# Performance work log

Measured on AMD Instinct MI355X. Metric: run time of the kernel, lower is better.

## Reference

```python
import math
import jax, jax.numpy as jnp
import numpy as np

N, C, H, W = 32, 64, 96, 96
SHIFT_H, SHIFT_W = 1, -1  # fixed values of the random roll shifts

def _dwconv(x, w, dilation, pad):
    # depthwise conv, x: (n,c,h,w), w: (c,1,kh,kw)
    return jax.lax.conv_general_dilated(
        x, w, window_strides=(1, 1), padding=((pad, pad), (pad, pad)),
        rhs_dilation=(dilation, dilation),
        dimension_numbers=('NCHW', 'OIHW', 'NCHW'),
        feature_group_count=x.shape[1])

def _unfold_1x7_d2(x):
    # F.unfold(x, (1,7), dilation=(1,2), padding=(0,6)) -> (n,c,7,h,w)
    n, c, h, w = x.shape
    xp = jnp.pad(x, ((0, 0), (0, 0), (0, 0), (6, 6)))
    return jnp.stack([xp[..., 2 * k: 2 * k + w] for k in range(7)], axis=2)

def setup_inputs() -> dict:
    key = jax.random.key(0)
    k0, k1, k2, k3, k4, k5 = jax.random.split(key, 6)
    std = 0.1
    return {
        'x':  jax.random.normal(k0, (N, C, H, W), dtype=jnp.float32),
        'w3': jax.random.normal(k1, (C, 1, 5, 5), dtype=jnp.float32) * std,
        'w4': jax.random.normal(k2, (C, 1, 3, 3), dtype=jnp.float32) * std,
        'p5': jax.random.normal(k3, (1, C, C), dtype=jnp.float32) * std,
        'p6': jax.random.normal(k4, (C, 1), dtype=jnp.float32) * std,
        'p8': jax.random.normal(k5, (C, C * 7), dtype=jnp.float32) * std,
    }

def reference(x, w3, w4, p5, p6, p8):
    n, c, h, w = x.shape
    hw = h * w
    t0 = x
    t1 = jnp.roll(jnp.roll(t0, SHIFT_H, axis=2), SHIFT_W, axis=3)
    # channel attention: (n,c,c)
    t2 = jnp.einsum('nci,ndi->ncd', t0.reshape(n, c, hw), t1.reshape(n, c, hw)) / math.sqrt(hw)
    t3 = _dwconv(t1, w3, dilation=1, pad=2)          # (n,c,h,w)
    t4 = _dwconv(t1, w4, dilation=2, pad=2)          # (n,c,h,w)
    t5 = p5 * t2                                      # (n,c,c)
    t6 = jnp.einsum('nchw,ce->nehw', t4, p6).reshape(n, h, w)
    t7 = _unfold_1x7_d2(t0).reshape(n, c * 7, hw)     # (n, c*7, hw)
    t8 = jnp.einsum('nbc,bd->ndc', t5, p8)            # (n, c*7, c)
    t9 = jnp.einsum('nci,ni->nc', t3.reshape(n, c, hw), t6.reshape(n, hw)) / math.sqrt(hw)
    t10 = jnp.einsum('nkc,nks->ncs', t8, t7) / math.sqrt(c * 7)  # (n,c,hw)
    t11 = t9[:, :, None] + t10
    return t11.reshape(n, c, h, w)
```

## Files before the change

### kernel.cpp

```cpp
#include <hip/hip_runtime.h>

#define NB 32
#define CCH 64
#define HH 96
#define WWID 96
#define HWP (HH*WWID)
#define K7 448

#define OFF_T5 2097152
#define OFF_T8 2228224
#define OFF_T6 3145728
#define OFF_T9 3440640

typedef __attribute__((ext_vector_type(8))) short short8;
typedef __attribute__((ext_vector_type(4))) float floatx4;

__device__ __forceinline__ short f2bf(float x) {
    unsigned u = __float_as_uint(x);
    unsigned r = (u + 0x7FFF + ((u >> 16) & 1)) >> 16;
    return (short)r;
}

__device__ __forceinline__ int roll_idx(int i) {
    int h = i / WWID;
    int w = i - h * WWID;
    return ((h + HH - 1) % HH) * WWID + ((w + 1) % WWID);
}

__global__ __launch_bounds__(256) void k_t2(const float* __restrict__ x,
                                            float* __restrict__ t2p) {
    int blk = blockIdx.x;
    int n = blk >> 4, sl = blk & 15;
    int k0 = sl * (HWP / 16);
    __shared__ float ash[32][68];
    __shared__ float bsh[32][68];
    int t = threadIdx.x;
    int c0 = (t >> 4) * 4;
    int d0 = (t & 15) * 4;
    float acc[4][4] = {};
    const float* xa = x + (size_t)n * CCH * HWP;

    for (int kc = 0; kc < 576; kc += 32) {
        __syncthreads();
#pragma unroll
        for (int i = 0; i < 8; i++) {
            int idx = i * 256 + t;
            int c = idx >> 5, kk = idx & 31;
            int gi = k0 + kc + kk;
            ash[kk][c] = xa[c * HWP + gi];
            bsh[kk][c] = xa[c * HWP + roll_idx(gi)];
        }
        __syncthreads();
#pragma unroll
        for (int kk = 0; kk < 32; kk++) {
            float4 va = *(const float4*)&ash[kk][c0];
            float4 vb = *(const float4*)&bsh[kk][d0];
            float av[4] = {va.x, va.y, va.z, va.w};
            float bv[4] = {vb.x, vb.y, vb.z, vb.w};
#pragma unroll
            for (int i = 0; i < 4; i++)
#pragma unroll
                for (int j = 0; j < 4; j++)
                    acc[i][j] = fmaf(av[i], bv[j], acc[i][j]);
        }
    }
    float* o = t2p + (((size_t)n * 16 + sl) * 64 + c0) * 64 + d0;
#pragma unroll
    for (int i = 0; i < 4; i++) {
        float4 v = {acc[i][0], acc[i][1], acc[i][2], acc[i][3]};
        *(float4*)(o + i * 64) = v;
    }
}

__global__ __launch_bounds__(256) void k_t5(const float* __restrict__ t2p,
                                            const float* __restrict__ p5,
                                            float* __restrict__ t5) {
    int idx = blockIdx.x * 256 + threadIdx.x;
    int n = idx >> 12, rc = idx & 4095;
    float s = 0.f;
#pragma unroll
    for (int sl = 0; sl < 16; sl++)
        s += t2p[((size_t)n * 16 + sl) * 4096 + rc];
    t5[idx] = s * p5[rc] * (1.0f / 96.0f);
}

__global__ __launch_bounds__(256) void k_t8(const float* __restrict__ t5,
                                            const float* __restrict__ p8,
                                            short* __restrict__ t8t) {
    int n = blockIdx.y;
    int idx = blockIdx.x * 256 + threadIdx.x;
    int k = idx >> 6, c = idx & 63;
    const float* t5n = t5 + (size_t)n * 4096;
    float s = 0.f;
#pragma unroll 8
    for (int b = 0; b < 64; b++)
        s += t5n[b * 64 + c] * p8[b * K7 + k];
    int c7 = k / 7, kk = k - c7 * 7;
    t8t[((size_t)n * 64 + c) * K7 + kk * 64 + c7] = f2bf(s * 0.04724555912f);
}

__global__ __launch_bounds__(256) void k_t6(const float* __restrict__ x,
                                            const float* __restrict__ w4,
                                            const float* __restrict__ p6,
                                            float* __restrict__ t6) {
    int n = blockIdx.y;
    int pix = blockIdx.x * 256 + threadIdx.x;
    int h = pix / WWID, w = pix - h * WWID;

    int off9[9];
    float m9[9];
#pragma unroll
    for (int i = 0; i < 3; i++) {
        int gh = h + (i - 1) * 2;
        bool vr = (gh >= 0) && (gh < HH);
        int srow = vr ? ((gh + HH - 1) % HH) * WWID : 0;
        float rm = vr ? 1.f : 0.f;
#pragma unroll
        for (int j = 0; j < 3; j++) {
            int gw = w + (j - 1) * 2;
            bool vc = (gw >= 0) && (gw < WWID);
            int scol = vc ? (gw + 1) % WWID : 0;
            off9[i * 3 + j] = srow + scol;
            m9[i * 3 + j] = vc ? rm : 0.f;
        }
    }
    const float* xn = x + (size_t)n * CCH * HWP;
    float acc = 0.f;
    for (int c = 0; c < CCH; c++) {
        const float* xc = xn + c * HWP;
        float pw = p6[c];
        const float* wc = w4 + c * 9;
#pragma unroll
        for (int ij = 0; ij < 9; ij++) {
            float wm = wc[ij] * pw * m9[ij];
            acc = fmaf(wm, xc[off9[ij]], acc);
        }
    }
    t6[(size_t)n * HWP + pix] = acc;
}

__global__ __launch_bounds__(256) void k_t9(const float* __restrict__ x,
                                            const float* __restrict__ w3,
                                            const float* __restrict__ t6,
                                            float* __restrict__ t9) {
    int n = blockIdx.y, c = blockIdx.x;
    __shared__ float xl[100][100];
    __shared__ float red[4];
    int t = threadIdx.x;
    const float* xc = x + ((size_t)n * CCH + c) * HWP;
    const float* t6n = t6 + (size_t)n * HWP;

    for (int idx = t; idx < 784; idx += 256) {
        if (idx < 400) {
            int r = idx / 100, col = idx - r * 100;
            int row = r < 2 ? r : r + 96;
            xl[row][col] = 0.f;
        } else {
            int rem = idx - 400;
            int h2 = rem >> 2, c4 = rem & 3;
            int col = c4 < 2 ? c4 : c4 + 96;
            xl[2 + h2][col] = 0.f;
        }
    }
    for (int idx = t; idx < HWP; idx += 256) {
        int h = idx / WWID, w = idx - h * WWID;
        int sh = (h == 0) ? (HH - 1) : (h - 1);
        int sw = (w == WWID - 1) ? 0 : (w + 1);
        xl[h + 2][w + 2] = xc[sh * WWID + sw];
    }
    float wv[25];
#pragma unroll
    for (int i = 0; i < 25; i++) wv[i] = w3[c * 25 + i];
    __syncthreads();

    float acc = 0.f;
#pragma unroll
    for (int g = 0; g < 9; g++) {
        int idx = g * 256 + t;
        int h = idx / 24, wg = idx - h * 24;
        int w0 = wg * 4;
        float4 tv = *(const float4*)(t6n + h * WWID + w0);
        float conv[4] = {0.f, 0.f, 0.f, 0.f};
#pragma unroll
        for (int kh = 0; kh < 5; kh++) {
            float4 ra = *(const float4*)&xl[h + kh][w0];
            float4 rb = *(const float4*)&xl[h + kh][w0 + 4];
            float r[8] = {ra.x, ra.y, ra.z, ra.w, rb.x, rb.y, rb.z, rb.w};
#pragma unroll
            for (int kw = 0; kw < 5; kw++) {
                float wk = wv[kh * 5 + kw];
                conv[0] = fmaf(wk, r[kw],     conv[0]);
                conv[1] = fmaf(wk, r[kw + 1], conv[1]);
                conv[2] = fmaf(wk, r[kw + 2], conv[2]);
                conv[3] = fmaf(wk, r[kw + 3], conv[3]);
            }
        }
        acc = fmaf(conv[0], tv.x, acc);
        acc = fmaf(conv[1], tv.y, acc);
        acc = fmaf(conv[2], tv.z, acc);
        acc = fmaf(conv[3], tv.w, acc);
    }
#pragma unroll
    for (int off = 32; off > 0; off >>= 1) acc += __shfl_down(acc, off, 64);
    if ((t & 63) == 0) red[t >> 6] = acc;
    __syncthreads();
    if (t == 0)
        t9[n * 64 + c] = (red[0] + red[1] + red[2] + red[3]) * (1.0f / 96.0f);
}

__global__ __launch_bounds__(256) void k_out(const float* __restrict__ x,
                                             const short* __restrict__ t8t,
                                             const float* __restrict__ t9,
                                             float* __restrict__ out) {
    int n = blockIdx.y;
    int h0 = blockIdx.x * 2;
    __shared__ short xsh[2 * 108 * 72];
    int t = threadIdx.x;

    for (int idx = t; idx < 2 * 12 * 72; idx += 256) {
        int r = idx / (12 * 72);
        int rem = idx - r * (12 * 72);
        int iwz = rem / 72, c7 = rem - iwz * 72;
        int iw = iwz < 6 ? iwz : iwz + 96;
        xsh[(r * 108 + iw) * 72 + c7] = 0;
    }
    const float* xn = x + (size_t)n * CCH * HWP;
    for (int idx = t; idx < 2 * CCH * WWID; idx += 256) {
        int r = idx / (CCH * WWID);
        int rem = idx - r * (CCH * WWID);
        int c7 = rem / WWID, w = rem - c7 * WWID;
        float v = xn[c7 * HWP + (h0 + r) * WWID + w];
        xsh[(r * 108 + w + 6) * 72 + c7] = f2bf(v);
    }
    __syncthreads();

    int lane = t & 63, wv = t >> 6;
    int q = lane >> 4, sl = lane & 15;
    floatx4 acc[4][3] = {};
    const short* A = t8t + (size_t)n * 64 * K7;

    for (int kc = 0; kc < K7; kc += 32) {
        int kk = kc >> 6;
        int c7b = (kc & 63) + q * 8;
        short8 a[4], b[3];
#pragma unroll
        for (int mi = 0; mi < 4; mi++)
            a[mi] = *(const short8*)(A + (mi * 16 + sl) * K7 + kc + q * 8);
#pragma unroll
        for (int sj = 0; sj < 3; sj++) {
            int si = wv * 3 + sj;
            int r = si >= 6 ? 1 : 0;
            int iw = (si - r * 6) * 16 + sl + 2 * kk;
            b[sj] = *(const short8*)&xsh[(r * 108 + iw) * 72 + c7b];
        }
#pragma unroll
        for (int mi = 0; mi < 4; mi++)
#pragma unroll
            for (int sj = 0; sj < 3; sj++)
                acc[mi][sj] = __builtin_amdgcn_mfma_f32_16x16x32_bf16(
                    a[mi], b[sj], acc[mi][sj], 0, 0, 0);
    }

    const float* t9n = t9 + n * 64;
#pragma unroll
    for (int mi = 0; mi < 4; mi++) {
#pragma unroll
        for (int i = 0; i < 4; i++) {
            int c = mi * 16 + q * 4 + i;
            float tv = t9n[c];
            float* orow = out + ((size_t)n * CCH + c) * HWP;
#pragma unroll
            for (int sj = 0; sj < 3; sj++) {
                int si = wv * 3 + sj;
                int r = si >= 6 ? 1 : 0;
                int w = (si - r * 6) * 16 + sl;
                orow[(h0 + r) * WWID + w] = acc[mi][sj][i] + tv;
            }
        }
    }
}

extern "C" void kernel_launch(void* const* d_in, const int* in_sizes, int n_in,
                              void* d_out, int out_size, void* d_ws, size_t ws_size,
                              hipStream_t stream) {
    const float* x  = (const float*)d_in[0];
    const float* w3 = (const float*)d_in[1];
    const float* w4 = (const float*)d_in[2];
    const float* p5 = (const float*)d_in[3];
    const float* p6 = (const float*)d_in[4];
    const float* p8 = (const float*)d_in[5];
    float* out = (float*)d_out;
    float* ws  = (float*)d_ws;

    float* t2p = ws;
    float* t5  = ws + OFF_T5;
    short* t8t = (short*)(ws + OFF_T8);
    float* t6  = ws + OFF_T6;
    float* t9  = ws + OFF_T9;

    k_t2<<<512, 256, 0, stream>>>(x, t2p);
    k_t5<<<512, 256, 0, stream>>>(t2p, p5, t5);
    k_t8<<<dim3(112, 32), 256, 0, stream>>>(t5, p8, t8t);
    k_t6<<<dim3(36, 32), 256, 0, stream>>>(x, w4, p6, t6);
    k_t9<<<dim3(64, 32), 256, 0, stream>>>(x, w3, t6, t9);
    k_out<<<dim3(48, 32), 256, 0, stream>>>(x, t8t, t9, out);
}
```

Measured before the change: 295.4 us.

## Use bf16 MFMA for channel attention and pre-transpose x to bf16 for output GEMM

Rewrites the t2 Gram-matrix kernel to read x directly from global memory, with the roll folded into the addressing, convert it to bf16 and accumulate with 16x16x32 MFMA instead of scalar fp32 FMAs through LDS. A new kernel transposes x once into a channel-last bf16 layout so the output GEMM can load B fragments straight from global memory. That removes the per-block LDS staging, the zero padding and the barrier. The cost is an extra launch, extra workspace traffic and lower precision for the t2 accumulation inputs.

Result: slower. 347.1 us (+17.5%).

```diff
diff --git a/kernel.cpp b/kernel.cpp
--- a/kernel.cpp
+++ b/kernel.cpp
@@ -9,8 +9,9 @@
 
 #define OFF_T5 2097152
 #define OFF_T8 2228224
-#define OFF_T6 3145728
-#define OFF_T9 3440640
+#define OFF_T6 2686976
+#define OFF_T9 2981888
+#define OFF_XT 2983936
 
 typedef __attribute__((ext_vector_type(8))) short short8;
 typedef __attribute__((ext_vector_type(4))) float floatx4;
@@ -21,55 +22,66 @@
     return (short)r;
 }
 
-__device__ __forceinline__ int roll_idx(int i) {
-    int h = i / WWID;
-    int w = i - h * WWID;
-    return ((h + HH - 1) % HH) * WWID + ((w + 1) % WWID);
+__global__ __launch_bounds__(256) void k_xt(const float* __restrict__ x,
+                                            short* __restrict__ xt) {
+    int n = blockIdx.y, h = blockIdx.x;
+    __shared__ float xl[64][97];
+    int t = threadIdx.x;
+    const float* xn = x + (size_t)n * CCH * HWP + h * WWID;
+#pragma unroll
+    for (int i = 0; i < 24; i++) {
+        int e = i * 256 + t;
+        int c = e / 96, w = e - c * 96;
+        xl[c][w] = xn[c * HWP + w];
+    }
+    __syncthreads();
+    short* xtn = xt + ((size_t)n * HH + h) * (WWID * 64);
+    int c = t & 63, wg = t >> 6;
+#pragma unroll
+    for (int i = 0; i < 24; i++) {
+        int w = i * 4 + wg;
+        xtn[w * 64 + c] = f2bf(xl[c][w]);
+    }
 }
 
 __global__ __launch_bounds__(256) void k_t2(const float* __restrict__ x,
                                             float* __restrict__ t2p) {
-    int blk = blockIdx.x;
-    int n = blk >> 4, sl = blk & 15;
-    int k0 = sl * (HWP / 16);
-    __shared__ float ash[32][68];
-    __shared__ float bsh[32][68];
+    int n = blockIdx.x >> 4, ks = blockIdx.x & 15;
     int t = threadIdx.x;
-    int c0 = (t >> 4) * 4;
-    int d0 = (t & 15) * 4;
-    float acc[4][4] = {};
-    const float* xa = x + (size_t)n * CCH * HWP;
-
-    for (int kc = 0; kc < 576; kc += 32) {
-        __syncthreads();
-#pragma unroll
-        for (int i = 0; i < 8; i++) {
-            int idx = i * 256 + t;
-            int c = idx >> 5, kk = idx & 31;
-            int gi = k0 + kc + kk;
-            ash[kk][c] = xa[c * HWP + gi];
-            bsh[kk][c] = xa[c * HWP + roll_idx(gi)];
-        }
-        __syncthreads();
-#pragma unroll
-        for (int kk = 0; kk < 32; kk++) {
-            float4 va = *(const float4*)&ash[kk][c0];
-            float4 vb = *(const float4*)&bsh[kk][d0];
-            float av[4] = {va.x, va.y, va.z, va.w};
-            float bv[4] = {vb.x, vb.y, vb.z, vb.w};
-#pragma unroll
-            for (int i = 0; i < 4; i++)
-#pragma unroll
-                for (int j = 0; j < 4; j++)
-                    acc[i][j] = fmaf(av[i], bv[j], acc[i][j]);
-        }
-    }
-    float* o = t2p + (((size_t)n * 16 + sl) * 64 + c0) * 64 + d0;
-#pragma unroll
-    for (int i = 0; i < 4; i++) {
-        float4 v = {acc[i][0], acc[i][1], acc[i][2], acc[i][3]};
-        *(float4*)(o + i * 64) = v;
-    }
+    int wv = t >> 6, lane = t & 63;
+    int q = lane >> 4, m = lane & 15;
+    const float* xn = x + (size_t)n * CCH * HWP;
+    const float* xa = xn + (wv * 16 + m) * HWP;
+    floatx4 acc[4] = {};
+
+    int k0 = ks * 576;
+    for (int kc = k0; kc < k0 + 576; kc += 32) {
+        int h = kc / 96;
+        int w0 = kc - h * 96;
+        int hr = (h == 0) ? (HH - 1) : (h - 1);
+        float4 a0 = *(const float4*)(xa + kc + q * 8);
+        float4 a1 = *(const float4*)(xa + kc + q * 8 + 4);
+        short8 af = {f2bf(a0.x), f2bf(a0.y), f2bf(a0.z), f2bf(a0.w),
+                     f2bf(a1.x), f2bf(a1.y), f2bf(a1.z), f2bf(a1.w)};
+#pragma unroll
+        for (int j = 0; j < 4; j++) {
+            const float* xr = xn + (j * 16 + m) * HWP + hr * 96;
+            int base = w0 + q * 8;
+            float4 b0 = *(const float4*)(xr + base);
+            float4 b1 = *(const float4*)(xr + base + 4);
+            int c8 = base + 8;
+            float e8 = xr[c8 == 96 ? 0 : c8];
+            short8 bf = {f2bf(b0.y), f2bf(b0.z), f2bf(b0.w), f2bf(b1.x),
+                         f2bf(b1.y), f2bf(b1.z), f2bf(b1.w), f2bf(e8)};
+            acc[j] = __builtin_amdgcn_mfma_f32_16x16x32_bf16(af, bf, acc[j], 0, 0, 0);
+        }
+    }
+    float* o = t2p + ((size_t)(n * 16 + ks)) * 4096;
+#pragma unroll
+    for (int j = 0; j < 4; j++)
+#pragma unroll
+        for (int i = 0; i < 4; i++)
+            o[(wv * 16 + q * 4 + i) * 64 + j * 16 + m] = acc[j][i];
 }
 
 __global__ __launch_bounds__(256) void k_t5(const float* __restrict__ t2p,
@@ -208,50 +220,41 @@
         t9[n * 64 + c] = (red[0] + red[1] + red[2] + red[3]) * (1.0f / 96.0f);
 }
 
-__global__ __launch_bounds__(256) void k_out(const float* __restrict__ x,
+__global__ __launch_bounds__(256) void k_out(const short* __restrict__ xt,
                                              const short* __restrict__ t8t,
                                              const float* __restrict__ t9,
                                              float* __restrict__ out) {
     int n = blockIdx.y;
     int h0 = blockIdx.x * 2;
-    __shared__ short xsh[2 * 108 * 72];
-    int t = threadIdx.x;
-
-    for (int idx = t; idx < 2 * 12 * 72; idx += 256) {
-        int r = idx / (12 * 72);
-        int rem = idx - r * (12 * 72);
-        int iwz = rem / 72, c7 = rem - iwz * 72;
-        int iw = iwz < 6 ? iwz : iwz + 96;
-        xsh[(r * 108 + iw) * 72 + c7] = 0;
-    }
-    const float* xn = x + (size_t)n * CCH * HWP;
-    for (int idx = t; idx < 2 * CCH * WWID; idx += 256) {
-        int r = idx / (CCH * WWID);
-        int rem = idx - r * (CCH * WWID);
-        int c7 = rem / WWID, w = rem - c7 * WWID;
-        float v = xn[c7 * HWP + (h0 + r) * WWID + w];
-        xsh[(r * 108 + w + 6) * 72 + c7] = f2bf(v);
-    }
-    __syncthreads();
-
-    int lane = t & 63, wv = t >> 6;
+    int t = threadIdx.x, lane = t & 63, wv = t >> 6;
     int q = lane >> 4, sl = lane & 15;
+
+    int sw[3], rr[3];
+#pragma unroll
+    for (int sj = 0; sj < 3; sj++) {
+        int si = wv * 3 + sj;
+        rr[sj] = (si >= 6) ? 1 : 0;
+        sw[sj] = (si - rr[sj] * 6) * 16 + sl;
+    }
+
     floatx4 acc[4][3] = {};
-    const short* A = t8t + (size_t)n * 64 * K7;
+    const short* A = t8t + (size_t)n * 64 * K7 + sl * K7 + q * 8;
+    const short* X0 = xt + ((size_t)n * HH + h0) * (WWID * 64);
 
     for (int kc = 0; kc < K7; kc += 32) {
         int kk = kc >> 6;
         int c7b = (kc & 63) + q * 8;
-        short8 a[4], b[3];
+        short8 a[4];
 #pragma unroll
         for (int mi = 0; mi < 4; mi++)
-            a[mi] = *(const short8*)(A + (mi * 16 + sl) * K7 + kc + q * 8);
+            a[mi] = *(const short8*)(A + mi * 16 * K7 + kc);
+        short8 b[3];
+        short8 bz = {};
 #pragma unroll
         for (int sj = 0; sj < 3; sj++) {
-            int si = wv * 3 + sj;
-            int r = si >= 6 ? 1 : 0;
-            int iw = (si - r * 6) * 16 + sl + 2 * kk;
-            b[sj] = *(const short8*)&xsh[(r * 108 + iw) * 72 + c7b];
+            int w = sw[sj] + 2 * kk - 6;
+            const short8* p = (const short8*)(X0 + ((size_t)(rr[sj] * WWID + w)) * 64 + c7b);
+            b[sj] = ((unsigned)w < 96u) ? *p : bz;
         }
 #pragma unroll
         for (int mi = 0; mi < 4; mi++)
@@ -268,14 +271,10 @@
         for (int i = 0; i < 4; i++) {
             int c = mi * 16 + q * 4 + i;
             float tv = t9n[c];
-            float* orow = out + ((size_t)n * CCH + c) * HWP;
-#pragma unroll
-            for (int sj = 0; sj < 3; sj++) {
-                int si = wv * 3 + sj;
-                int r = si >= 6 ? 1 : 0;
-                int w = (si - r * 6) * 16 + sl;
-                orow[(h0 + r) * WWID + w] = acc[mi][sj][i] + tv;
-            }
+            float* orow = out + ((size_t)n * CCH + c) * HWP + h0 * WWID;
+#pragma unroll
+            for (int sj = 0; sj < 3; sj++)
+                orow[rr[sj] * WWID + sw[sj]] = acc[mi][sj][i] + tv;
         }
     }
 }
@@ -297,11 +296,13 @@
     short* t8t = (short*)(ws + OFF_T8);
     float* t6  = ws + OFF_T6;
     float* t9  = ws + OFF_T9;
-
+    short* xt  = (short*)(ws + OFF_XT);
+
+    k_xt<<<dim3(96, 32), 256, 0, stream>>>(x, xt);
     k_t2<<<512, 256, 0, stream>>>(x, t2p);
     k_t5<<<512, 256, 0, stream>>>(t2p, p5, t5);
     k_t8<<<dim3(112, 32), 256, 0, stream>>>(t5, p8, t8t);
     k_t6<<<dim3(36, 32), 256, 0, stream>>>(x, w4, p6, t6);
     k_t9<<<dim3(64, 32), 256, 0, stream>>>(x, w3, t6, t9);
-    k_out<<<dim3(48, 32), 256, 0, stream>>>(x, t8t, t9, out);
-}
+    k_out<<<dim3(48, 32), 256, 0, stream>>>(xt, t8t, t9, out);
+}
```
